# Performance work log

Measured on AMD Instinct MI355X. Metric: run time of the kernel, lower is better.

## Reference

```python
import jax, jax.numpy as jnp
import numpy as np

N_NODES = 100000
N_EDGES = 1600000
IN_DIM = 128
HID_DIM = 128
N_MASK = 5000
N_CLASSES = 4


def gcn_layer(x, src, dst, edge_weight, W, b):
    """PyG GCNConv: x' = D^{-1/2} (A + I) D^{-1/2} (x W) + b, with edge weights."""
    n = x.shape[0]
    loop = jnp.arange(n, dtype=src.dtype)
    s = jnp.concatenate([src, loop])                      # [E+N]
    d = jnp.concatenate([dst, loop])                      # [E+N]
    w = jnp.concatenate([edge_weight, jnp.ones((n,), edge_weight.dtype)])
    deg = jax.ops.segment_sum(w, d, num_segments=n)       # weighted in-degree incl. self-loop
    dis = jnp.where(deg > 0, jax.lax.rsqrt(deg), 0.0)     # deg^{-1/2}, inf -> 0
    norm = dis[s] * w * dis[d]                            # [E+N]
    h = x @ W                                             # [N, H] small GEMM
    msg = h[s] * norm[:, None]                            # gather + scale  [E+N, H]
    out = jax.ops.segment_sum(msg, d, num_segments=n)     # scatter-add     [N, H]
    return out + b


def setup_inputs() -> dict:
    key = jax.random.key(0)
    ks = jax.random.split(key, 8)
    x = jax.random.normal(ks[0], (N_NODES, IN_DIM), dtype=jnp.float32)
    edge_weight = jax.random.uniform(ks[1], (N_EDGES,), dtype=jnp.float32)
    W1 = jax.random.normal(ks[2], (IN_DIM, HID_DIM), dtype=jnp.float32) * (1.0 / np.sqrt(IN_DIM))
    b1 = jnp.zeros((HID_DIM,), jnp.float32)
    W2 = jax.random.normal(ks[3], (HID_DIM, HID_DIM), dtype=jnp.float32) * (1.0 / np.sqrt(HID_DIM))
    b2 = jnp.zeros((HID_DIM,), jnp.float32)
    edge_index = jax.random.randint(ks[4], (2, N_EDGES), 0, N_NODES, dtype=jnp.int32)
    mask_idx = jax.random.randint(ks[5], (N_MASK,), 0, N_NODES, dtype=jnp.int32)
    y = jax.random.randint(ks[6], (N_NODES,), 0, N_CLASSES, dtype=jnp.int32)
    return {"x": x, "edge_weight": edge_weight, "W1": W1, "b1": b1,
            "W2": W2, "b2": b2, "edge_index": edge_index,
            "mask_idx": mask_idx, "y": y}


def reference(x, edge_weight, W1, b1, W2, b2, edge_index, mask_idx, y):
    src, dst = edge_index[0], edge_index[1]
    h = gcn_layer(x, src, dst, edge_weight, W1, b1)
    h = jax.nn.relu(h)
    # F.dropout(training=False) in eval mode is identity
    h = gcn_layer(h, src, dst, edge_weight, W2, b2)
    return h[mask_idx], y[mask_idx]
```

## Files before the change

kernel.cpp:

```cpp
#include <hip/hip_runtime.h>

constexpr int N = 100000;
constexpr int E = 1600000;
constexpr int D = 128;
constexpr int M = 5000;

constexpr int MF_BLKS = (N + 255) / 256;

constexpr int NBITS = 7;
constexpr int BUCKET = 1 << NBITS;
constexpr int NB  = (N + BUCKET - 1) / BUCKET;
constexpr int CAP = 3072;
constexpr int EBP = 4096;
constexpr int NPP = (E + EBP - 1) / EBP;
constexpr int PREP_BLKS = 32;
constexpr int MB_BLKS = (M + 255) / 256;

typedef __attribute__((ext_vector_type(8))) short bf16x8;
typedef __attribute__((ext_vector_type(4))) float f32x4;


__device__ __forceinline__ unsigned int pack_bf16x2(float a, float b) {
    unsigned int ua = __float_as_uint(a);
    unsigned int ub = __float_as_uint(b);
    ua = (ua + 0x7FFFu + ((ua >> 16) & 1u)) >> 16;
    ub = (ub + 0x7FFFu + ((ub >> 16) & 1u)) & 0xFFFF0000u;
    return ua | ub;
}
__device__ __forceinline__ unsigned short bf16_rne(float a) {
    unsigned int ua = __float_as_uint(a);
    return (unsigned short)((ua + 0x7FFFu + ((ua >> 16) & 1u)) >> 16);
}
__device__ __forceinline__ float bf16_lo(unsigned int u) { return __uint_as_float(u << 16); }
__device__ __forceinline__ float bf16_hi(unsigned int u) { return __uint_as_float(u & 0xFFFF0000u); }


__global__ __launch_bounds__(256) void k_misc0(const float* __restrict__ W1,
                                               unsigned int* __restrict__ Wt1,
                                               const int* __restrict__ mask,
                                               unsigned int* __restrict__ maskbit,
                                               unsigned int* __restrict__ needed) {
    const int t = threadIdx.x;
    if (blockIdx.x < PREP_BLKS) {
        int idx = blockIdx.x * 256 + t;
        int n = idx >> 6, kk = idx & 63;
        float a = W1[(2 * kk) * D + n];
        float b = W1[(2 * kk + 1) * D + n];
        Wt1[idx] = pack_bf16x2(a, b);
    } else {
        int i = (blockIdx.x - PREP_BLKS) * 256 + t;
        if (i < M) {
            int n = mask[i];
            atomicOr(&maskbit[n >> 5], 1u << (n & 31));
            atomicOr(&needed[n >> 5], 1u << (n & 31));
        }
    }
}


__global__ __launch_bounds__(1024) void k_part(const int* __restrict__ src,
                                               const int* __restrict__ dst,
                                               const float* __restrict__ ew,
                                               int* __restrict__ gCursor,
                                               unsigned long long* __restrict__ tmp,
                                               const unsigned int* __restrict__ maskbit,
                                               unsigned int* __restrict__ needed) {
    __shared__ int cnt[NB];
    __shared__ int off[NB];
    __shared__ int rk[NB];
    const int t = threadIdx.x;
    for (int i = t; i < NB; i += 1024) { cnt[i] = 0; rk[i] = 0; }
    __syncthreads();

    const int eb = blockIdx.x * EBP;
    int d_[4], s_[4];
    float w_[4];
#pragma unroll
    for (int i = 0; i < 4; ++i) {
        int e = eb + t + i * 1024;
        if (e < E) {
            d_[i] = __builtin_nontemporal_load(dst + e);
            s_[i] = __builtin_nontemporal_load(src + e);
            w_[i] = __builtin_nontemporal_load(ew + e);
            atomicAdd(&cnt[d_[i] >> NBITS], 1);
        } else {
            d_[i] = -1;
        }
    }
    __syncthreads();

    for (int i = t; i < NB; i += 1024) {
        int c = cnt[i];
        if (c > 0) off[i] = atomicAdd(&gCursor[i], c);
    }
    __syncthreads();

#pragma unroll
    for (int i = 0; i < 4; ++i) {
        if (d_[i] >= 0) {
            int b = d_[i] >> NBITS;
            int r = atomicAdd(&rk[b], 1);
            int posr = off[b] + r;
            if (posr < CAP) {
                unsigned long long rec =
                    ((unsigned long long)(unsigned int)__float_as_int(w_[i]) << 32) |
                    ((unsigned int)s_[i] << NBITS) | (unsigned int)(d_[i] & (BUCKET - 1));
                tmp[(size_t)b * CAP + posr] = rec;
            }
            if ((maskbit[d_[i] >> 5] >> (d_[i] & 31)) & 1u)
                atomicOr(&needed[s_[i] >> 5], 1u << (s_[i] & 31));
        }
    }
}


union SMem {
    unsigned int Ws[128 * 68];
    float wsumL[BUCKET];
};


__device__ __forceinline__ void gemm_mfma_body(unsigned int* __restrict__ Ws,
                                               const float* __restrict__ Xin,
                                               const unsigned int* __restrict__ Wt,
                                               unsigned short* __restrict__ out, int blk) {
    const int t = threadIdx.x;
#pragma unroll
    for (int i = 0; i < 8; ++i) {
        int f4 = t + i * 256;
        int n = f4 >> 4;
        int k4 = f4 & 15;
        uint4 w = ((const uint4*)Wt)[f4];
        *(uint4*)(&Ws[n * 68 + k4 * 4]) = w;
    }
    __syncthreads();

    const int wv = t >> 6, lane = t & 63;
    const int q = lane >> 4, l15 = lane & 15;
    const int rowBase = blk * 256 + wv * 64;

    f32x4 acc[4][8] = {};
#pragma unroll
    for (int kc = 0; kc < 4; ++kc) {
        bf16x8 af[4];
#pragma unroll
        for (int rt = 0; rt < 4; ++rt) {
            int row = rowBase + rt * 16 + l15;
            if (row > N - 1) row = N - 1;
            union { uint4 u; bf16x8 v; } cv;
            const float* xr = Xin + (size_t)row * D + kc * 32 + q * 8;
            float4 x0 = *(const float4*)xr;
            float4 x1 = *(const float4*)(xr + 4);
            cv.u.x = pack_bf16x2(x0.x, x0.y);
            cv.u.y = pack_bf16x2(x0.z, x0.w);
            cv.u.z = pack_bf16x2(x1.x, x1.y);
            cv.u.w = pack_bf16x2(x1.z, x1.w);
            af[rt] = cv.v;
        }
#pragma unroll
        for (int ct = 0; ct < 8; ++ct) {
            union { uint4 u; bf16x8 v; } bv;
            bv.u = *(const uint4*)(&Ws[(ct * 16 + l15) * 68 + kc * 16 + q * 4]);
#pragma unroll
            for (int rt = 0; rt < 4; ++rt)
                acc[rt][ct] = __builtin_amdgcn_mfma_f32_16x16x32_bf16(af[rt], bv.v, acc[rt][ct], 0, 0, 0);
        }
    }

#pragma unroll
    for (int rt = 0; rt < 4; ++rt) {
#pragma unroll
        for (int ct = 0; ct < 8; ++ct) {
            int col = ct * 16 + l15;
#pragma unroll
            for (int r = 0; r < 4; ++r) {
                int row = rowBase + rt * 16 + q * 4 + r;
                if (row < N) out[(size_t)row * D + col] = bf16_rne(acc[rt][ct][r]);
            }
        }
    }
}


__global__ __launch_bounds__(256) void k_disA_g1(const unsigned long long* __restrict__ tmp,
                                                 const int* __restrict__ gCursor,
                                                 float* __restrict__ dis,
                                                 const float* __restrict__ x,
                                                 const unsigned int* __restrict__ Wt1,
                                                 unsigned short* __restrict__ A) {
    __shared__ SMem sm;
    const int t = threadIdx.x;
    if (blockIdx.x < NB) {
        const int bk = blockIdx.x;
        if (t < BUCKET) sm.wsumL[t] = 0.f;
        __syncthreads();
        const size_t segBeg = (size_t)bk * CAP;
        int segLen = gCursor[bk];
        if (segLen > CAP) segLen = CAP;
        for (int e = t; e < segLen; e += 256) {
            unsigned long long rec = tmp[segBeg + e];
            atomicAdd(&sm.wsumL[(int)(rec & (BUCKET - 1))],
                      __uint_as_float((unsigned int)(rec >> 32)));
        }
        __syncthreads();
        if (t < BUCKET) {
            int node = bk * BUCKET + t;
            if (node < N) dis[node] = rsqrtf(1.0f + sm.wsumL[t]);
        }
    } else {
        gemm_mfma_body(sm.Ws, x, Wt1, A, blockIdx.x - NB);
    }
}


__global__ __launch_bounds__(512) void k_sort_agg(const unsigned long long* __restrict__ tmp,
                                                  const int* __restrict__ gCursor,
                                                  const float* __restrict__ dis,
                                                  const unsigned int* __restrict__ needed,
                                                  const unsigned int* __restrict__ maskbit,
                                                  const float* __restrict__ b,
                                                  const unsigned int* __restrict__ Hb,
                                                  int* __restrict__ rowStart,
                                                  int* __restrict__ rowLen,
                                                  int2* __restrict__ pairs,
                                                  unsigned int* __restrict__ outB) {
    __shared__ int2 lp[CAP];
    __shared__ int cnt[BUCKET];
    __shared__ int offL[BUCKET + 1];
    __shared__ int wl[BUCKET];
    __shared__ int waveS[2];
    __shared__ int nw, wcur;
    const int bk = blockIdx.x;
    const int t = threadIdx.x;
    const size_t segBeg = (size_t)bk * CAP;
    int segLen = gCursor[bk];
    if (segLen > CAP) segLen = CAP;

    if (t == 0) { nw = 0; wcur = 0; offL[BUCKET] = segLen; }
    if (t < BUCKET) cnt[t] = 0;
    const uint4 mb4 = ((const uint4*)maskbit)[bk];
    __syncthreads();

    unsigned long long r_[6];
#pragma unroll
    for (int i = 0; i < 6; ++i) {
        int e = t + i * 512;
        if (e < segLen) {
            r_[i] = tmp[segBeg + e];
            atomicAdd(&cnt[(int)(r_[i] & (BUCKET - 1))], 1);
        }
    }
    __syncthreads();

    const int lane = t & 63;
    {
        const int wv2 = t >> 6;
        const int pv = (t < BUCKET) ? cnt[t] : 0;
        int v = pv;
        for (int o = 1; o < 64; o <<= 1) {
            int u = __shfl_up(v, o);
            if (lane >= o) v += u;
        }
        if (lane == 63 && wv2 < 2) waveS[wv2] = v;
        __syncthreads();
        if (t < BUCKET) {
            const int wb = (wv2 == 1) ? waveS[0] : 0;
            const int ex = wb + v - pv;
            offL[t] = ex;
            const int node = bk * BUCKET + t;
            if (node < N) {
                rowStart[node] = (int)segBeg + ex;
                rowLen[node] = pv;
                if ((needed[node >> 5] >> (node & 31)) & 1u) {
                    int r = atomicAdd(&nw, 1);
                    wl[r] = t;
                }
            }
            cnt[t] = 0;
        }
    }
    __syncthreads();

#pragma unroll
    for (int i = 0; i < 6; ++i) {
        int e = t + i * 512;
        if (e < segLen) {
            unsigned long long rec = r_[i];
            int dl = (int)(rec & (BUCKET - 1));
            int s  = (int)((rec >> NBITS) & 0xFFFFF);
            float w = __uint_as_float((unsigned int)(rec >> 32));
            float v = w * dis[s];
            int r = atomicAdd(&cnt[dl], 1);
            int pos = offL[dl] + r;
            int2 pr = make_int2(s, __float_as_int(v));
            lp[pos] = pr;
            unsigned int mw = (dl < 32) ? mb4.x : (dl < 64) ? mb4.y : (dl < 96) ? mb4.z : mb4.w;
            if ((mw >> (dl & 31)) & 1u) pairs[segBeg + pos] = pr;
        }
    }
    __syncthreads();

    for (;;) {
        int idx;
        if (lane == 0) idx = atomicAdd(&wcur, 1);
        idx = __shfl(idx, 0);
        if (idx >= nw) break;
        const int nl = wl[idx];
        const int node = bk * BUCKET + nl;
        const int beg = offL[nl], end = offL[nl + 1];
        float ax = 0.f, ay = 0.f;
        int j = beg;
        for (; j + 7 < end; j += 8) {
            int2 p[8];
            unsigned int h[8];
#pragma unroll
            for (int i = 0; i < 8; ++i) p[i] = lp[j + i];
#pragma unroll
            for (int i = 0; i < 8; ++i) h[i] = Hb[(size_t)p[i].x * 64 + lane];
#pragma unroll
            for (int i = 0; i < 8; ++i) {
                float v = __int_as_float(p[i].y);
                ax += bf16_lo(h[i]) * v;
                ay += bf16_hi(h[i]) * v;
            }
        }
        for (; j < end; ++j) {
            int2 p0 = lp[j];
            unsigned int h0 = Hb[(size_t)p0.x * 64 + lane];
            float v0 = __int_as_float(p0.y);
            ax += bf16_lo(h0) * v0;
            ay += bf16_hi(h0) * v0;
        }
        float dd = dis[node];
        float sn = dd * dd;
        unsigned int hs = Hb[(size_t)node * 64 + lane];
        float2 bb = ((const float2*)b)[lane];
        float ox = fmaxf(ax * dd + bf16_lo(hs) * sn + bb.x, 0.f);
        float oy = fmaxf(ay * dd + bf16_hi(hs) * sn + bb.y, 0.f);
        __builtin_nontemporal_store(pack_bf16x2(ox, oy), outB + (size_t)node * 64 + lane);
    }
}


__global__ __launch_bounds__(256) void k_mask_out(const unsigned int* __restrict__ Hb,
                                                  const int2* __restrict__ pairs,
                                                  const int* __restrict__ rowStart,
                                                  const int* __restrict__ rowLen,
                                                  const float* __restrict__ dis,
                                                  const float* __restrict__ W2,
                                                  const float* __restrict__ b2,
                                                  const int* __restrict__ mask,
                                                  const int* __restrict__ y,
                                                  float* __restrict__ out) {
    __shared__ float w2s[64 * 132];
    __shared__ float rowL[4][128];
    const int t = threadIdx.x;
    const int wv = t >> 6, lane = t & 63;
    const int i = blockIdx.x * 4 + wv;
    const int node = mask[i];
    const int beg = rowStart[node], end = beg + rowLen[node];

    float ax = 0.f, ay = 0.f;
    int j = beg;
    for (; j + 7 < end; j += 8) {
        int2 p[8];
        unsigned int h[8];
#pragma unroll
        for (int ii = 0; ii < 8; ++ii) p[ii] = pairs[j + ii];
#pragma unroll
        for (int ii = 0; ii < 8; ++ii) h[ii] = Hb[(size_t)p[ii].x * 64 + lane];
#pragma unroll
        for (int ii = 0; ii < 8; ++ii) {
            float v = __int_as_float(p[ii].y);
            ax += bf16_lo(h[ii]) * v;
            ay += bf16_hi(h[ii]) * v;
        }
    }
    for (; j < end; ++j) {
        int2 p0 = pairs[j];
        unsigned int h0 = Hb[(size_t)p0.x * 64 + lane];
        float v0 = __int_as_float(p0.y);
        ax += bf16_lo(h0) * v0;
        ay += bf16_hi(h0) * v0;
    }
    {
        float dd = dis[node];
        float sn = dd * dd;
        unsigned int hs = Hb[(size_t)node * 64 + lane];
        rowL[wv][2 * lane]     = ax * dd + bf16_lo(hs) * sn;
        rowL[wv][2 * lane + 1] = ay * dd + bf16_hi(hs) * sn;
    }

    float2 bb = ((const float2*)b2)[lane];
    float acc0 = bb.x, acc1 = bb.y;
#pragma unroll
    for (int h0 = 0; h0 < 2; ++h0) {
        __syncthreads();
        for (int idx = t; idx < 2048; idx += 256) {
            float4 v = ((const float4*)W2)[h0 * 2048 + idx];
            int k = (idx * 4) >> 7, n = (idx * 4) & 127;
            *(float4*)(&w2s[k * 132 + n]) = v;
        }
        __syncthreads();
#pragma unroll 8
        for (int k = 0; k < 64; ++k) {
            float a = rowL[wv][h0 * 64 + k];
            float2 w = *(const float2*)(&w2s[k * 132 + 2 * lane]);
            acc0 += a * w.x;
            acc1 += a * w.y;
        }
    }
    ((float2*)(out + (size_t)i * D))[lane] = make_float2(acc0, acc1);
    if (lane == 0) out[(size_t)M * D + i] = (float)y[node];
}

extern "C" void kernel_launch(void* const* d_in, const int* in_sizes, int n_in,
                              void* d_out, int out_size, void* d_ws, size_t ws_size,
                              hipStream_t stream) {
    const float* x  = (const float*)d_in[0];
    const float* ew = (const float*)d_in[1];
    const float* W1 = (const float*)d_in[2];
    const float* b1 = (const float*)d_in[3];
    const float* W2 = (const float*)d_in[4];
    const float* b2 = (const float*)d_in[5];
    const int* eidx = (const int*)d_in[6];
    const int* mask = (const int*)d_in[7];
    const int* y    = (const int*)d_in[8];
    const int* src = eidx;
    const int* dst = eidx + E;

    char* ws = (char*)d_ws;
    float* dis      = (float*)(ws);
    int*   rowStart = (int*)(ws + (size_t)512 * 1024);
    int*   rowLen   = (int*)(ws + (size_t)1024 * 1024);
    unsigned int* maskbit = (unsigned int*)(ws + (size_t)1440 * 1024);
    unsigned int* needed  = (unsigned int*)(ws + (size_t)1456 * 1024);
    int*   gCursor  = (int*)(ws + (size_t)1472 * 1024);
    unsigned int* Wt1 = (unsigned int*)(ws + (size_t)1480 * 1024);
    int2*  pairs    = (int2*)(ws + (size_t)2 * 1024 * 1024);
    unsigned long long* tmp = (unsigned long long*)(ws + (size_t)22 * 1024 * 1024);
    unsigned short* A  = (unsigned short*)(ws + (size_t)42 * 1024 * 1024);
    unsigned short* B  = (unsigned short*)(ws + (size_t)68 * 1024 * 1024);

    (void)hipMemsetAsync(ws + (size_t)1440 * 1024, 0, (size_t)36 * 1024, stream);

    hipLaunchKernelGGL(k_misc0, dim3(PREP_BLKS + MB_BLKS), dim3(256), 0, stream,
                       W1, Wt1, mask, maskbit, needed);

    hipLaunchKernelGGL(k_part, dim3(NPP), dim3(1024), 0, stream,
                       src, dst, ew, gCursor, tmp, maskbit, needed);

    hipLaunchKernelGGL(k_disA_g1, dim3(NB + MF_BLKS), dim3(256), 0, stream,
                       tmp, gCursor, dis, x, Wt1, A);

    hipLaunchKernelGGL(k_sort_agg, dim3(NB), dim3(512), 0, stream,
                       tmp, gCursor, dis, needed, maskbit, b1,
                       (const unsigned int*)A, rowStart, rowLen, pairs, (unsigned int*)B);

    hipLaunchKernelGGL(k_mask_out, dim3(M / 4), dim3(256), 0, stream,
                       (const unsigned int*)B, pairs, rowStart, rowLen, dis, W2, b2,
                       mask, y, (float*)d_out);
}
```

Before: 238.7 us.

## Fold mask/weight prep kernel into partition kernel and widen sort-agg blocks

Removes the separate k_misc0 launch by adding extra blocks to k_part that do the W1 transpose/pack and set the mask bits. Each partition block now rebuilds the mask bitmap in shared memory from the mask indices, so it no longer depends on a global maskbit written by an earlier kernel. k_sort_agg moves from 512 to 1024 threads with fewer records per thread. The cost is 5000 redundant shared atomics per partition block plus 16KB of extra shared memory, which may reduce occupancy. The larger sort-agg blocks may also change the occupancy and register balance.

Result: no change. 237.4 us (-0.6%).

```diff
diff --git a/kernel.cpp b/kernel.cpp
--- a/kernel.cpp
+++ b/kernel.cpp
@@ -13,8 +13,9 @@
 constexpr int CAP = 3072;
 constexpr int EBP = 4096;
 constexpr int NPP = (E + EBP - 1) / EBP;
-constexpr int PREP_BLKS = 32;
-constexpr int MB_BLKS = (M + 255) / 256;
+constexpr int PREP_BLKS = 8;
+constexpr int MB_BLKS = (M + 1023) / 1024;
+constexpr int MBW = 4096;
 
 typedef __attribute__((ext_vector_type(8))) short bf16x8;
 typedef __attribute__((ext_vector_type(4))) float f32x4;
@@ -35,42 +36,51 @@
 __device__ __forceinline__ float bf16_hi(unsigned int u) { return __uint_as_float(u & 0xFFFF0000u); }
 
 
-__global__ __launch_bounds__(256) void k_misc0(const float* __restrict__ W1,
-                                               unsigned int* __restrict__ Wt1,
-                                               const int* __restrict__ mask,
-                                               unsigned int* __restrict__ maskbit,
-                                               unsigned int* __restrict__ needed) {
-    const int t = threadIdx.x;
-    if (blockIdx.x < PREP_BLKS) {
-        int idx = blockIdx.x * 256 + t;
-        int n = idx >> 6, kk = idx & 63;
-        float a = W1[(2 * kk) * D + n];
-        float b = W1[(2 * kk + 1) * D + n];
-        Wt1[idx] = pack_bf16x2(a, b);
-    } else {
-        int i = (blockIdx.x - PREP_BLKS) * 256 + t;
-        if (i < M) {
-            int n = mask[i];
-            atomicOr(&maskbit[n >> 5], 1u << (n & 31));
-            atomicOr(&needed[n >> 5], 1u << (n & 31));
-        }
-    }
-}
-
-
 __global__ __launch_bounds__(1024) void k_part(const int* __restrict__ src,
                                                const int* __restrict__ dst,
                                                const float* __restrict__ ew,
                                                int* __restrict__ gCursor,
                                                unsigned long long* __restrict__ tmp,
-                                               const unsigned int* __restrict__ maskbit,
-                                               unsigned int* __restrict__ needed) {
+                                               const int* __restrict__ mask,
+                                               unsigned int* __restrict__ maskbit,
+                                               unsigned int* __restrict__ needed,
+                                               const float* __restrict__ W1,
+                                               unsigned int* __restrict__ Wt1) {
     __shared__ int cnt[NB];
     __shared__ int off[NB];
     __shared__ int rk[NB];
+    __shared__ unsigned int mbit[MBW];
     const int t = threadIdx.x;
+
+    if (blockIdx.x >= NPP) {
+        const int bi = blockIdx.x - NPP;
+        if (bi < PREP_BLKS) {
+            int idx = bi * 1024 + t;
+            if (idx < 8192) {
+                int n = idx >> 6, kk = idx & 63;
+                float a = W1[(2 * kk) * D + n];
+                float b = W1[(2 * kk + 1) * D + n];
+                Wt1[idx] = pack_bf16x2(a, b);
+            }
+        } else {
+            int i = (bi - PREP_BLKS) * 1024 + t;
+            if (i < M) {
+                int n = mask[i];
+                atomicOr(&maskbit[n >> 5], 1u << (n & 31));
+                atomicOr(&needed[n >> 5], 1u << (n & 31));
+            }
+        }
+        return;
+    }
+
     for (int i = t; i < NB; i += 1024) { cnt[i] = 0; rk[i] = 0; }
-    __syncthreads();
+    for (int i = t; i < MBW; i += 1024) mbit[i] = 0;
+    __syncthreads();
+
+    for (int i = t; i < M; i += 1024) {
+        int n = mask[i];
+        atomicOr(&mbit[n >> 5], 1u << (n & 31));
+    }
 
     const int eb = blockIdx.x * EBP;
     int d_[4], s_[4];
@@ -107,7 +117,7 @@
                     ((unsigned int)s_[i] << NBITS) | (unsigned int)(d_[i] & (BUCKET - 1));
                 tmp[(size_t)b * CAP + posr] = rec;
             }
-            if ((maskbit[d_[i] >> 5] >> (d_[i] & 31)) & 1u)
+            if ((mbit[d_[i] >> 5] >> (d_[i] & 31)) & 1u)
                 atomicOr(&needed[s_[i] >> 5], 1u << (s_[i] & 31));
         }
     }
@@ -213,17 +223,17 @@
 }
 
 
-__global__ __launch_bounds__(512) void k_sort_agg(const unsigned long long* __restrict__ tmp,
-                                                  const int* __restrict__ gCursor,
-                                                  const float* __restrict__ dis,
-                                                  const unsigned int* __restrict__ needed,
-                                                  const unsigned int* __restrict__ maskbit,
-                                                  const float* __restrict__ b,
-                                                  const unsigned int* __restrict__ Hb,
-                                                  int* __restrict__ rowStart,
-                                                  int* __restrict__ rowLen,
-                                                  int2* __restrict__ pairs,
-                                                  unsigned int* __restrict__ outB) {
+__global__ __launch_bounds__(1024) void k_sort_agg(const unsigned long long* __restrict__ tmp,
+                                                   const int* __restrict__ gCursor,
+                                                   const float* __restrict__ dis,
+                                                   const unsigned int* __restrict__ needed,
+                                                   const unsigned int* __restrict__ maskbit,
+                                                   const float* __restrict__ b,
+                                                   const unsigned int* __restrict__ Hb,
+                                                   int* __restrict__ rowStart,
+                                                   int* __restrict__ rowLen,
+                                                   int2* __restrict__ pairs,
+                                                   unsigned int* __restrict__ outB) {
     __shared__ int2 lp[CAP];
     __shared__ int cnt[BUCKET];
     __shared__ int offL[BUCKET + 1];
@@ -241,10 +251,10 @@
     const uint4 mb4 = ((const uint4*)maskbit)[bk];
     __syncthreads();
 
-    unsigned long long r_[6];
-#pragma unroll
-    for (int i = 0; i < 6; ++i) {
-        int e = t + i * 512;
+    unsigned long long r_[3];
+#pragma unroll
+    for (int i = 0; i < 3; ++i) {
+        int e = t + i * 1024;
         if (e < segLen) {
             r_[i] = tmp[segBeg + e];
             atomicAdd(&cnt[(int)(r_[i] & (BUCKET - 1))], 1);
@@ -282,8 +292,8 @@
     __syncthreads();
 
 #pragma unroll
-    for (int i = 0; i < 6; ++i) {
-        int e = t + i * 512;
+    for (int i = 0; i < 3; ++i) {
+        int e = t + i * 1024;
         if (e < segLen) {
             unsigned long long rec = r_[i];
             int dl = (int)(rec & (BUCKET - 1));
@@ -444,16 +454,13 @@
 
     (void)hipMemsetAsync(ws + (size_t)1440 * 1024, 0, (size_t)36 * 1024, stream);
 
-    hipLaunchKernelGGL(k_misc0, dim3(PREP_BLKS + MB_BLKS), dim3(256), 0, stream,
-                       W1, Wt1, mask, maskbit, needed);
-
-    hipLaunchKernelGGL(k_part, dim3(NPP), dim3(1024), 0, stream,
-                       src, dst, ew, gCursor, tmp, maskbit, needed);
+    hipLaunchKernelGGL(k_part, dim3(NPP + PREP_BLKS + MB_BLKS), dim3(1024), 0, stream,
+                       src, dst, ew, gCursor, tmp, mask, maskbit, needed, W1, Wt1);
 
     hipLaunchKernelGGL(k_disA_g1, dim3(NB + MF_BLKS), dim3(256), 0, stream,
                        tmp, gCursor, dis, x, Wt1, A);
 
-    hipLaunchKernelGGL(k_sort_agg, dim3(NB), dim3(512), 0, stream,
+    hipLaunchKernelGGL(k_sort_agg, dim3(NB), dim3(1024), 0, stream,
                        tmp, gCursor, dis, needed, maskbit, b1,
                        (const unsigned int*)A, rowStart, rowLen, pairs, (unsigned int*)B);
 
```
